# Kernel optimization log

Hardware: AMD Instinct MI355X
Metric: run time of the kernel (lower is better)

Reference implementation:

```python
import jax, jax.numpy as jnp
import numpy as np

E = 1024      # embed_dim (== embed_dim_)
NH = 8        # num_heads
HD = E // NH  # head_dim
BS1 = 2048
BS2 = 2048
EPS = 1e-5


def _layernorm(x, g, b):
    m = jnp.mean(x, axis=-1, keepdims=True)
    v = jnp.mean(jnp.square(x - m), axis=-1, keepdims=True)
    return (x - m) * jax.lax.rsqrt(v + EPS) * g + b


def setup_inputs() -> dict:
    key = jax.random.key(0)
    ks = jax.random.split(key, 16)
    s = 1.0 / np.sqrt(E)
    s4 = 1.0 / np.sqrt(4 * E)
    inp = {
        "x1": jax.random.normal(ks[0], (BS1, E), jnp.float32),
        "x2": jax.random.normal(ks[1], (BS2, E), jnp.float32),
        "Wq": jax.random.uniform(ks[2], (E, E), jnp.float32, -s, s),
        "bq": jax.random.uniform(ks[3], (E,), jnp.float32, -s, s),
        "Wk": jax.random.uniform(ks[4], (E, E), jnp.float32, -s, s),
        "bk": jax.random.uniform(ks[5], (E,), jnp.float32, -s, s),
        "Wv": jax.random.uniform(ks[6], (E, E), jnp.float32, -s, s),
        "bv": jax.random.uniform(ks[7], (E,), jnp.float32, -s, s),
        "Wo": jax.random.uniform(ks[8], (E, E), jnp.float32, -s, s),
        "bo": jax.random.uniform(ks[9], (E,), jnp.float32, -s, s),
        "W1": jax.random.uniform(ks[10], (4 * E, E), jnp.float32, -s, s),
        "b1": jax.random.uniform(ks[11], (4 * E,), jnp.float32, -s, s),
        "W2": jax.random.uniform(ks[12], (E, 4 * E), jnp.float32, -s4, s4),
        "b2": jax.random.uniform(ks[13], (E,), jnp.float32, -s4, s4),
        "g1": jnp.ones((E,), jnp.float32),
        "be1": jnp.zeros((E,), jnp.float32),
        "g2": jnp.ones((E,), jnp.float32),
        "be2": jnp.zeros((E,), jnp.float32),
    }
    return inp


def reference(x1, x2, Wq, bq, Wk, bk, Wv, bv, Wo, bo, W1, b1, W2, b2, g1, be1, g2, be2):
    scale = HD ** -0.5
    # Projections; attention runs over the batch axis (n=bs1, m=bs2)
    q = (x1 @ Wq.T + bq).reshape(BS1, NH, HD)   # [n,h,d]
    k = (x2 @ Wk.T + bk).reshape(BS2, NH, HD)   # [m,h,d]
    v = (x2 @ Wv.T + bv).reshape(BS2, NH, HD)   # [m,h,d]
    scores = jnp.einsum('nhd,mhd->nmh', q, k) * scale  # [n,m,h]
    # NOTE: faithful to source: softmax over the HEADS axis (dim=-1)
    probs = jax.nn.softmax(scores, axis=-1)
    # dropout is identity in eval mode
    attn = jnp.einsum('nmh,mhd->nhd', probs, v).reshape(BS1, E)
    attn = attn @ Wo.T + bo
    h = _layernorm(x1 + attn, g1, be1)
    ffn = jax.nn.relu(h @ W1.T + b1) @ W2.T + b2
    return _layernorm(h + ffn, g2, be2)
```

## Files before the change

### kernel.cpp

```cpp
#include <hip/hip_runtime.h>

#define BS 2048
#define EMB 1024
#define NHEAD 8
#define HDIM 128

typedef unsigned short u16;
typedef __attribute__((ext_vector_type(8))) short bf16x8;
typedef __attribute__((ext_vector_type(4))) float f32x4;

__device__ __forceinline__ u16 f32_bf16(float f) {
  unsigned u = __float_as_uint(f);
  u += 0x7fffu + ((u >> 16) & 1u);
  return (u16)(u >> 16);
}
__device__ __forceinline__ float bf2f(u16 x) {
  return __uint_as_float((unsigned)x << 16);
}

__device__ __forceinline__ void gld_lds16(const void* g, void* l) {
  __builtin_amdgcn_global_load_lds(
      (const __attribute__((address_space(1))) void*)g,
      (__attribute__((address_space(3))) void*)l, 16, 0, 0);
}

struct CvtArgs { const float* src[8]; };
__global__ __launch_bounds__(256) void cvt_all(CvtArgs a, u16* __restrict__ dst) {
  long i = (long)blockIdx.x * 256 + threadIdx.x;
  int seg = (int)(i >> 18);
  const float* src; long b;
  if (seg < 2)       { src = a.src[0]; b = 0; }
  else if (seg < 4)  { src = a.src[1]; b = 2L << 18; }
  else if (seg == 4) { src = a.src[2]; b = 4L << 18; }
  else if (seg == 5) { src = a.src[3]; b = 5L << 18; }
  else if (seg == 6) { src = a.src[4]; b = 6L << 18; }
  else if (seg == 7) { src = a.src[5]; b = 7L << 18; }
  else if (seg < 12) { src = a.src[6]; b = 8L << 18; }
  else               { src = a.src[7]; b = 12L << 18; }
  float4 v = ((const float4*)src)[i - b];
  ushort4 o;
  o.x = f32_bf16(v.x); o.y = f32_bf16(v.y); o.z = f32_bf16(v.z); o.w = f32_bf16(v.w);
  ((ushort4*)dst)[i] = o;
}

__device__ __forceinline__ void gemm_core(
    const u16* __restrict__ A, const u16* __restrict__ B, void* __restrict__ Cp,
    const float* __restrict__ bias, int K, int lda, int ldb, int ldc,
    long cbase, int mode, int relu, int m0, int n0) {
  __shared__ __align__(16) u16 As[128 * 32];
  __shared__ __align__(16) u16 Bs[128 * 32];
  const int t = threadIdx.x;
  const int lane = t & 63, l15 = lane & 15, quad = lane >> 4;
  const int wv = t >> 6, wr = wv & 1, wc = wv >> 1;
  const int wbase = t & ~63;

  f32x4 acc[4][4];
#pragma unroll
  for (int r = 0; r < 4; ++r)
#pragma unroll
    for (int c = 0; c < 4; ++c) acc[r][c] = (f32x4){0.f, 0.f, 0.f, 0.f};

  for (int k0 = 0; k0 < K; k0 += 32) {
#pragma unroll
    for (int i = 0; i < 2; ++i) {
      int s = i * 256 + t;
      gld_lds16(A + (long)(m0 + (s >> 2)) * lda + k0 + (s & 3) * 8,
                As + (i * 256 + wbase) * 8);
    }
#pragma unroll
    for (int i = 0; i < 2; ++i) {
      int s = i * 256 + t;
      gld_lds16(B + (long)(n0 + (s >> 2)) * ldb + k0 + (s & 3) * 8,
                Bs + (i * 256 + wbase) * 8);
    }
    __syncthreads();
    bf16x8 fa[4], fb[4];
#pragma unroll
    for (int r = 0; r < 4; ++r)
      fa[r] = *(const bf16x8*)&As[(wr * 64 + r * 16 + l15) * 32 + quad * 8];
#pragma unroll
    for (int c = 0; c < 4; ++c)
      fb[c] = *(const bf16x8*)&Bs[(wc * 64 + c * 16 + l15) * 32 + quad * 8];
#pragma unroll
    for (int r = 0; r < 4; ++r)
#pragma unroll
      for (int c = 0; c < 4; ++c)
        acc[r][c] = __builtin_amdgcn_mfma_f32_16x16x32_bf16(fa[r], fb[c], acc[r][c], 0, 0, 0);
    __syncthreads();
  }

#pragma unroll
  for (int r = 0; r < 4; ++r)
#pragma unroll
    for (int c = 0; c < 4; ++c) {
      const int m = m0 + wr * 64 + r * 16 + quad * 4;
      const int n = n0 + wc * 64 + c * 16 + l15;
      const float bv = bias ? bias[n] : 0.f;
      f32x4 v = acc[r][c];
      if (mode == 2) {
        ushort4 o;
        o.x = f32_bf16(v[0] + bv);
        o.y = f32_bf16(v[1] + bv);
        o.z = f32_bf16(v[2] + bv);
        o.w = f32_bf16(v[3] + bv);
        *(ushort4*)((u16*)Cp + cbase + (long)n * ldc + m) = o;
      } else {
#pragma unroll
        for (int i = 0; i < 4; ++i) {
          float x = v[i] + bv;
          if (relu) x = fmaxf(x, 0.f);
          if (mode == 0)
            ((float*)Cp)[cbase + (long)(m + i) * ldc + n] = x;
          else
            ((u16*)Cp)[cbase + (long)(m + i) * ldc + n] = f32_bf16(x);
        }
      }
    }
}

__global__ __launch_bounds__(256) void gemm_bt_k(
    const u16* __restrict__ A, const u16* __restrict__ B, void* __restrict__ C,
    const float* __restrict__ bias, int K, int lda, int ldb, int ldc,
    long aOffZ, long bOffZ, long cOffZ, int mode, int relu) {
  gemm_core(A + (long)blockIdx.z * aOffZ, B + (long)blockIdx.z * bOffZ, C, bias,
            K, lda, ldb, ldc, (long)blockIdx.z * cOffZ, mode, relu,
            blockIdx.y * 128, blockIdx.x * 128);
}

__global__ __launch_bounds__(256) void qkv_kernel(
    const u16* __restrict__ x1b, const u16* __restrict__ x2b,
    const u16* __restrict__ Wqb, const u16* __restrict__ Wkb, const u16* __restrict__ Wvb,
    const float* __restrict__ bq, const float* __restrict__ bk, const float* __restrict__ bv,
    u16* __restrict__ Qb, u16* __restrict__ Kb, u16* __restrict__ Vt) {
  const int z = blockIdx.z;
  const u16* A = (z == 0) ? x1b : x2b;
  const u16* B = (z == 0) ? Wqb : (z == 1) ? Wkb : Wvb;
  void* C = (z == 0) ? (void*)Qb : (z == 1) ? (void*)Kb : (void*)Vt;
  const float* bias = (z == 0) ? bq : (z == 1) ? bk : bv;
  const int mode = (z == 2) ? 2 : 1;
  const int ldc = (z == 2) ? 2048 : 1024;
  gemm_core(A, B, C, bias, 1024, 1024, 1024, ldc, 0, mode, 0,
            blockIdx.y * 128, blockIdx.x * 128);
}

__global__ __launch_bounds__(512, 2) void attn_fused(
    const u16* __restrict__ Q, const u16* __restrict__ Km, const u16* __restrict__ Vt,
    u16* __restrict__ p0, u16* __restrict__ p1, u16* __restrict__ p2, u16* __restrict__ p3) {
  __shared__ __align__(16) u16 Qs[32 * 1024];
  __shared__ __align__(16) u16 Ps[8 * 32 * 128];
  const int t = threadIdx.x;
  const int lane = t & 63, l15 = lane & 15, quad = lane >> 4;
  const int w = t >> 6, wbase = t & ~63;
  const int n0 = blockIdx.x * 32;
  const int mz = blockIdx.y * 512;
  u16* part = (blockIdx.y == 0) ? p0 : (blockIdx.y == 1) ? p1 : (blockIdx.y == 2) ? p2 : p3;

#pragma unroll
  for (int i = 0; i < 8; ++i) {
    int s = i * 512 + t;
    int n = s >> 7;
    int kel = (((s & 127) << 3) ^ ((n & 7) << 3));
    gld_lds16(Q + (long)(n0 + n) * 1024 + kel, Qs + (i * 512 + wbase) * 8);
  }

  f32x4 accp[2][8];
#pragma unroll
  for (int r = 0; r < 2; ++r)
#pragma unroll
    for (int c = 0; c < 8; ++c) accp[r][c] = (f32x4){0.f, 0.f, 0.f, 0.f};

  for (int it = 0; it < 4; ++it) {
    __syncthreads();
    f32x4 accs[8][2];
#pragma unroll
    for (int h = 0; h < 8; ++h)
#pragma unroll
      for (int c = 0; c < 2; ++c) accs[h][c] = (f32x4){0.f, 0.f, 0.f, 0.f};
    const u16* krow = Km + (long)(mz + it * 128 + w * 16 + l15) * 1024;
#pragma unroll
    for (int h = 0; h < 8; ++h)
#pragma unroll
      for (int kk = 0; kk < 4; ++kk) {
        bf16x8 kf = *(const bf16x8*)&krow[h * 128 + kk * 32 + quad * 8];
#pragma unroll
        for (int c = 0; c < 2; ++c) {
          int n = c * 16 + l15;
          int kel = (h * 128 + kk * 32 + quad * 8) ^ ((n & 7) << 3);
          bf16x8 qf = *(const bf16x8*)&Qs[n * 1024 + kel];
          accs[h][c] = __builtin_amdgcn_mfma_f32_16x16x32_bf16(kf, qf, accs[h][c], 0, 0, 0);
        }
      }
    const float scale = 0.08838834764831845f;
#pragma unroll
    for (int c = 0; c < 2; ++c)
#pragma unroll
      for (int i = 0; i < 4; ++i) {
        float mx = accs[0][c][i];
#pragma unroll
        for (int h = 1; h < 8; ++h) mx = fmaxf(mx, accs[h][c][i]);
        float sum = 0.f;
#pragma unroll
        for (int h = 0; h < 8; ++h) {
          float e = __expf((accs[h][c][i] - mx) * scale);
          accs[h][c][i] = e;
          sum += e;
        }
        float inv = 1.f / sum;
#pragma unroll
        for (int h = 0; h < 8; ++h) accs[h][c][i] *= inv;
      }
#pragma unroll
    for (int h = 0; h < 8; ++h)
#pragma unroll
      for (int c = 0; c < 2; ++c) {
        int n = c * 16 + l15;
        ushort4 o;
        o.x = f32_bf16(accs[h][c][0]);
        o.y = f32_bf16(accs[h][c][1]);
        o.z = f32_bf16(accs[h][c][2]);
        o.w = f32_bf16(accs[h][c][3]);
        int mb = (w * 32 + quad * 8) ^ ((n & 7) << 4);
        *(ushort4*)((char*)Ps + h * 8192 + n * 256 + mb) = o;
      }
    __syncthreads();
#pragma unroll
    for (int mq = 0; mq < 4; ++mq) {
      bf16x8 pa[2];
#pragma unroll
      for (int r = 0; r < 2; ++r) {
        int n = r * 16 + l15;
        int mb = (mq * 64 + quad * 16) ^ ((n & 7) << 4);
        pa[r] = *(const bf16x8*)((const char*)Ps + w * 8192 + n * 256 + mb);
      }
#pragma unroll
      for (int c = 0; c < 8; ++c) {
        bf16x8 vf = *(const bf16x8*)&Vt[(long)(w * 128 + c * 16 + l15) * 2048 +
                                        mz + it * 128 + mq * 32 + quad * 8];
#pragma unroll
        for (int r = 0; r < 2; ++r)
          accp[r][c] = __builtin_amdgcn_mfma_f32_16x16x32_bf16(pa[r], vf, accp[r][c], 0, 0, 0);
      }
    }
  }
#pragma unroll
  for (int r = 0; r < 2; ++r)
#pragma unroll
    for (int c = 0; c < 8; ++c)
#pragma unroll
      for (int i = 0; i < 4; ++i)
        part[(long)(n0 + r * 16 + quad * 4 + i) * 1024 + w * 128 + c * 16 + l15] =
            f32_bf16(accp[r][c][i]);
}

__global__ __launch_bounds__(256) void reduce4p_bf16(
    const u16* __restrict__ p0, const u16* __restrict__ p1,
    const u16* __restrict__ p2, const u16* __restrict__ p3, u16* __restrict__ out) {
  long i = (long)blockIdx.x * 256 + threadIdx.x;
  ushort4 a = ((const ushort4*)p0)[i];
  ushort4 b = ((const ushort4*)p1)[i];
  ushort4 c = ((const ushort4*)p2)[i];
  ushort4 d = ((const ushort4*)p3)[i];
  ushort4 o;
  o.x = f32_bf16(bf2f(a.x) + bf2f(b.x) + bf2f(c.x) + bf2f(d.x));
  o.y = f32_bf16(bf2f(a.y) + bf2f(b.y) + bf2f(c.y) + bf2f(d.y));
  o.z = f32_bf16(bf2f(a.z) + bf2f(b.z) + bf2f(c.z) + bf2f(d.z));
  o.w = f32_bf16(bf2f(a.w) + bf2f(b.w) + bf2f(c.w) + bf2f(d.w));
  ((ushort4*)out)[i] = o;
}

__global__ __launch_bounds__(256) void ln_residual_p4(
    const float* __restrict__ x,
    const u16* __restrict__ p0, const u16* __restrict__ p1,
    const u16* __restrict__ p2, const u16* __restrict__ p3,
    const float* __restrict__ colb, const float* __restrict__ g, const float* __restrict__ b,
    float* __restrict__ out32, u16* __restrict__ out16) {
  const int row = blockIdx.x, t = threadIdx.x;
  const long base = (long)row * EMB;
  float4 v = ((const float4*)(x + base))[t];
  ushort4 a0 = ((const ushort4*)(p0 + base))[t];
  ushort4 a1 = ((const ushort4*)(p1 + base))[t];
  ushort4 a2 = ((const ushort4*)(p2 + base))[t];
  ushort4 a3 = ((const ushort4*)(p3 + base))[t];
  float4 cb = ((const float4*)colb)[t];
  v.x += bf2f(a0.x) + bf2f(a1.x) + bf2f(a2.x) + bf2f(a3.x) + cb.x;
  v.y += bf2f(a0.y) + bf2f(a1.y) + bf2f(a2.y) + bf2f(a3.y) + cb.y;
  v.z += bf2f(a0.z) + bf2f(a1.z) + bf2f(a2.z) + bf2f(a3.z) + cb.z;
  v.w += bf2f(a0.w) + bf2f(a1.w) + bf2f(a2.w) + bf2f(a3.w) + cb.w;
  float s = v.x + v.y + v.z + v.w;
  float q = v.x * v.x + v.y * v.y + v.z * v.z + v.w * v.w;
#pragma unroll
  for (int off = 32; off > 0; off >>= 1) {
    s += __shfl_xor(s, off);
    q += __shfl_xor(q, off);
  }
  __shared__ float red[8];
  const int wv = t >> 6, lane = t & 63;
  if (lane == 0) { red[wv] = s; red[4 + wv] = q; }
  __syncthreads();
  s = red[0] + red[1] + red[2] + red[3];
  q = red[4] + red[5] + red[6] + red[7];
  const float mean = s * (1.f / EMB);
  const float var = q * (1.f / EMB) - mean * mean;
  const float rstd = rsqrtf(var + 1e-5f);
  float4 gg = ((const float4*)g)[t];
  float4 bb = ((const float4*)b)[t];
  float4 o;
  o.x = (v.x - mean) * rstd * gg.x + bb.x;
  o.y = (v.y - mean) * rstd * gg.y + bb.y;
  o.z = (v.z - mean) * rstd * gg.z + bb.z;
  o.w = (v.w - mean) * rstd * gg.w + bb.w;
  ((float4*)(out32 + base))[t] = o;
  if (out16) {
    ushort4 ho;
    ho.x = f32_bf16(o.x); ho.y = f32_bf16(o.y); ho.z = f32_bf16(o.z); ho.w = f32_bf16(o.w);
    ((ushort4*)(out16 + base))[t] = ho;
  }
}

extern "C" void kernel_launch(void* const* d_in, const int* in_sizes, int n_in,
                              void* d_out, int out_size, void* d_ws, size_t ws_size,
                              hipStream_t stream) {
  const float* x1 = (const float*)d_in[0];
  const float* x2 = (const float*)d_in[1];
  const float* Wq = (const float*)d_in[2];
  const float* bq = (const float*)d_in[3];
  const float* Wk = (const float*)d_in[4];
  const float* bk = (const float*)d_in[5];
  const float* Wv = (const float*)d_in[6];
  const float* bv = (const float*)d_in[7];
  const float* Wo = (const float*)d_in[8];
  const float* bo = (const float*)d_in[9];
  const float* W1 = (const float*)d_in[10];
  const float* b1 = (const float*)d_in[11];
  const float* W2 = (const float*)d_in[12];
  const float* b2 = (const float*)d_in[13];
  const float* g1 = (const float*)d_in[14];
  const float* be1 = (const float*)d_in[15];
  const float* g2 = (const float*)d_in[16];
  const float* be2 = (const float*)d_in[17];

  char* ws = (char*)d_ws;
  const size_t MB = 1ull << 20;
  u16* x1b = (u16*)(ws + 0 * MB);
  u16* x2b = (u16*)(ws + 4 * MB);
  u16* Wqb = (u16*)(ws + 8 * MB);
  u16* Wkb = (u16*)(ws + 10 * MB);
  u16* Wvb = (u16*)(ws + 12 * MB);
  u16* Wob = (u16*)(ws + 14 * MB);
  u16* W1b = (u16*)(ws + 16 * MB);
  u16* W2b = (u16*)(ws + 24 * MB);
  u16* Qb  = (u16*)(ws + 32 * MB);
  u16* Kb  = (u16*)(ws + 36 * MB);
  u16* Vtb = (u16*)(ws + 40 * MB);
  u16* attnb = (u16*)(ws + 44 * MB);
  u16* aP[4] = {(u16*)(ws + 48 * MB), (u16*)(ws + 52 * MB),
                (u16*)(ws + 56 * MB), (u16*)(ws + 60 * MB)};
  u16* woP[4] = {(u16*)(ws + 48 * MB), (u16*)(ws + 52 * MB),
                 (u16*)(ws + 56 * MB), (u16*)(ws + 60 * MB)};
  float* h32  = (float*)(ws + 64 * MB);
  u16*  h16   = (u16*)(ws + 72 * MB);
  u16*  ffn1b = (u16*)(ws + 76 * MB);
  u16* f2P[4] = {(u16*)(ws + 92 * MB), (u16*)(ws + 96 * MB),
                 (u16*)(ws + 100 * MB), (u16*)(ws + 104 * MB)};

  CvtArgs ca;
  ca.src[0] = x1; ca.src[1] = x2; ca.src[2] = Wq; ca.src[3] = Wk;
  ca.src[4] = Wv; ca.src[5] = Wo; ca.src[6] = W1; ca.src[7] = W2;
  cvt_all<<<16384, 256, 0, stream>>>(ca, (u16*)ws);

  qkv_kernel<<<dim3(8, 16, 3), 256, 0, stream>>>(x1b, x2b, Wqb, Wkb, Wvb, bq, bk, bv, Qb, Kb, Vtb);

  attn_fused<<<dim3(64, 4), 512, 0, stream>>>(Qb, Kb, Vtb, aP[0], aP[1], aP[2], aP[3]);

  reduce4p_bf16<<<2048, 256, 0, stream>>>(aP[0], aP[1], aP[2], aP[3], attnb);

  gemm_bt_k<<<dim3(8, 16, 4), 256, 0, stream>>>(attnb, Wob, woP[0], nullptr,
                                                256, 1024, 1024, 1024,
                                                256, 256, (long)BS * 1024, 1, 0);

  ln_residual_p4<<<2048, 256, 0, stream>>>(x1, woP[0], woP[1], woP[2], woP[3],
                                           bo, g1, be1, h32, h16);

  gemm_bt_k<<<dim3(32, 16, 1), 256, 0, stream>>>(h16, W1b, ffn1b, b1,
                                                 1024, 1024, 1024, 4096,
                                                 0, 0, 0, 1, 1);

  gemm_bt_k<<<dim3(8, 16, 4), 256, 0, stream>>>(ffn1b, W2b, f2P[0], nullptr,
                                                1024, 4096, 4096, 1024,
                                                1024, 1024, (long)BS * 1024, 1, 0);

  ln_residual_p4<<<2048, 256, 0, stream>>>(h32, f2P[0], f2P[1], f2P[2], f2P[3],
                                           b2, g2, be2, (float*)d_out, nullptr);
}
```

Measured before the change: 336.4 us.

## Split attention n-rows across twice as many waves per block

Launches the fused attention kernel with 1024 threads, so each of 16 waves handles 16 query rows for one m-slice instead of 32 rows. This halves per-wave accumulator registers and doubles waves per CU to improve latency hiding. In exchange, K and V fragments are fetched redundantly by both row-halves, and the aggressive launch bound may constrain register allocation.

```diff
diff --git a/kernel.cpp b/kernel.cpp
--- a/kernel.cpp
+++ b/kernel.cpp
@@ -143,7 +143,7 @@
             blockIdx.y * 128, blockIdx.x * 128);
 }
 
-__global__ __launch_bounds__(512, 2) void attn_fused(
+__global__ __launch_bounds__(1024, 4) void attn_fused(
     const u16* __restrict__ Q, const u16* __restrict__ Km, const u16* __restrict__ Vt,
     u16* __restrict__ p0, u16* __restrict__ p1, u16* __restrict__ p2, u16* __restrict__ p3) {
   __shared__ __align__(16) u16 Qs[32 * 1024];
@@ -151,105 +151,86 @@
   const int t = threadIdx.x;
   const int lane = t & 63, l15 = lane & 15, quad = lane >> 4;
   const int w = t >> 6, wbase = t & ~63;
+  const int mw = w & 7, nh = w >> 3;
   const int n0 = blockIdx.x * 32;
   const int mz = blockIdx.y * 512;
   u16* part = (blockIdx.y == 0) ? p0 : (blockIdx.y == 1) ? p1 : (blockIdx.y == 2) ? p2 : p3;
 
 #pragma unroll
-  for (int i = 0; i < 8; ++i) {
-    int s = i * 512 + t;
+  for (int i = 0; i < 4; ++i) {
+    int s = i * 1024 + t;
     int n = s >> 7;
     int kel = (((s & 127) << 3) ^ ((n & 7) << 3));
-    gld_lds16(Q + (long)(n0 + n) * 1024 + kel, Qs + (i * 512 + wbase) * 8);
-  }
-
-  f32x4 accp[2][8];
-#pragma unroll
-  for (int r = 0; r < 2; ++r)
-#pragma unroll
-    for (int c = 0; c < 8; ++c) accp[r][c] = (f32x4){0.f, 0.f, 0.f, 0.f};
+    gld_lds16(Q + (long)(n0 + n) * 1024 + kel, Qs + (i * 1024 + wbase) * 8);
+  }
+
+  const int nq = nh * 16 + l15;
+  const int swz3 = (nq & 7) << 3;
+  const int swz4 = (nq & 7) << 4;
+
+  f32x4 accp[8];
+#pragma unroll
+  for (int c = 0; c < 8; ++c) accp[c] = (f32x4){0.f, 0.f, 0.f, 0.f};
 
   for (int it = 0; it < 4; ++it) {
     __syncthreads();
-    f32x4 accs[8][2];
-#pragma unroll
-    for (int h = 0; h < 8; ++h)
-#pragma unroll
-      for (int c = 0; c < 2; ++c) accs[h][c] = (f32x4){0.f, 0.f, 0.f, 0.f};
-    const u16* krow = Km + (long)(mz + it * 128 + w * 16 + l15) * 1024;
+    f32x4 accs[8];
+#pragma unroll
+    for (int h = 0; h < 8; ++h) accs[h] = (f32x4){0.f, 0.f, 0.f, 0.f};
+    const u16* krow = Km + (long)(mz + it * 128 + mw * 16 + l15) * 1024;
 #pragma unroll
     for (int h = 0; h < 8; ++h)
 #pragma unroll
       for (int kk = 0; kk < 4; ++kk) {
         bf16x8 kf = *(const bf16x8*)&krow[h * 128 + kk * 32 + quad * 8];
-#pragma unroll
-        for (int c = 0; c < 2; ++c) {
-          int n = c * 16 + l15;
-          int kel = (h * 128 + kk * 32 + quad * 8) ^ ((n & 7) << 3);
-          bf16x8 qf = *(const bf16x8*)&Qs[n * 1024 + kel];
-          accs[h][c] = __builtin_amdgcn_mfma_f32_16x16x32_bf16(kf, qf, accs[h][c], 0, 0, 0);
-        }
+        bf16x8 qf = *(const bf16x8*)&Qs[nq * 1024 + ((h * 128 + kk * 32 + quad * 8) ^ swz3)];
+        accs[h] = __builtin_amdgcn_mfma_f32_16x16x32_bf16(kf, qf, accs[h], 0, 0, 0);
       }
     const float scale = 0.08838834764831845f;
 #pragma unroll
-    for (int c = 0; c < 2; ++c)
-#pragma unroll
-      for (int i = 0; i < 4; ++i) {
-        float mx = accs[0][c][i];
-#pragma unroll
-        for (int h = 1; h < 8; ++h) mx = fmaxf(mx, accs[h][c][i]);
-        float sum = 0.f;
-#pragma unroll
-        for (int h = 0; h < 8; ++h) {
-          float e = __expf((accs[h][c][i] - mx) * scale);
-          accs[h][c][i] = e;
-          sum += e;
-        }
-        float inv = 1.f / sum;
-#pragma unroll
-        for (int h = 0; h < 8; ++h) accs[h][c][i] *= inv;
+    for (int i = 0; i < 4; ++i) {
+      float mx = accs[0][i];
+#pragma unroll
+      for (int h = 1; h < 8; ++h) mx = fmaxf(mx, accs[h][i]);
+      float sum = 0.f;
+#pragma unroll
+      for (int h = 0; h < 8; ++h) {
+        float e = __expf((accs[h][i] - mx) * scale);
+        accs[h][i] = e;
+        sum += e;
       }
-#pragma unroll
-    for (int h = 0; h < 8; ++h)
-#pragma unroll
-      for (int c = 0; c < 2; ++c) {
-        int n = c * 16 + l15;
-        ushort4 o;
-        o.x = f32_bf16(accs[h][c][0]);
-        o.y = f32_bf16(accs[h][c][1]);
-        o.z = f32_bf16(accs[h][c][2]);
-        o.w = f32_bf16(accs[h][c][3]);
-        int mb = (w * 32 + quad * 8) ^ ((n & 7) << 4);
-        *(ushort4*)((char*)Ps + h * 8192 + n * 256 + mb) = o;
+      float inv = 1.f / sum;
+#pragma unroll
+      for (int h = 0; h < 8; ++h) accs[h][i] *= inv;
+    }
+#pragma unroll
+    for (int h = 0; h < 8; ++h) {
+      ushort4 o;
+      o.x = f32_bf16(accs[h][0]);
+      o.y = f32_bf16(accs[h][1]);
+      o.z = f32_bf16(accs[h][2]);
+      o.w = f32_bf16(accs[h][3]);
+      *(ushort4*)((char*)Ps + h * 8192 + nq * 256 + ((mw * 32 + quad * 8) ^ swz4)) = o;
+    }
+    __syncthreads();
+#pragma unroll
+    for (int mq = 0; mq < 4; ++mq) {
+      bf16x8 pa = *(const bf16x8*)((const char*)Ps + mw * 8192 + nq * 256 +
+                                   ((mq * 64 + quad * 16) ^ swz4));
+      const u16* vb = Vt + (long)(mw * 128) * 2048 + mz + it * 128 + mq * 32 + quad * 8;
+#pragma unroll
+      for (int c = 0; c < 8; ++c) {
+        bf16x8 vf = *(const bf16x8*)&vb[(long)(c * 16 + l15) * 2048];
+        accp[c] = __builtin_amdgcn_mfma_f32_16x16x32_bf16(pa, vf, accp[c], 0, 0, 0);
       }
-    __syncthreads();
-#pragma unroll
-    for (int mq = 0; mq < 4; ++mq) {
-      bf16x8 pa[2];
-#pragma unroll
-      for (int r = 0; r < 2; ++r) {
-        int n = r * 16 + l15;
-        int mb = (mq * 64 + quad * 16) ^ ((n & 7) << 4);
-        pa[r] = *(const bf16x8*)((const char*)Ps + w * 8192 + n * 256 + mb);
-      }
-#pragma unroll
-      for (int c = 0; c < 8; ++c) {
-        bf16x8 vf = *(const bf16x8*)&Vt[(long)(w * 128 + c * 16 + l15) * 2048 +
-                                        mz + it * 128 + mq * 32 + quad * 8];
-#pragma unroll
-        for (int r = 0; r < 2; ++r)
-          accp[r][c] = __builtin_amdgcn_mfma_f32_16x16x32_bf16(pa[r], vf, accp[r][c], 0, 0, 0);
-      }
-    }
-  }
-#pragma unroll
-  for (int r = 0; r < 2; ++r)
-#pragma unroll
-    for (int c = 0; c < 8; ++c)
-#pragma unroll
-      for (int i = 0; i < 4; ++i)
-        part[(long)(n0 + r * 16 + quad * 4 + i) * 1024 + w * 128 + c * 16 + l15] =
-            f32_bf16(accp[r][c][i]);
+    }
+  }
+#pragma unroll
+  for (int c = 0; c < 8; ++c)
+#pragma unroll
+    for (int i = 0; i < 4; ++i)
+      part[(long)(n0 + nh * 16 + quad * 4 + i) * 1024 + mw * 128 + c * 16 + l15] =
+          f32_bf16(accp[c][i]);
 }
 
 __global__ __launch_bounds__(256) void reduce4p_bf16(
@@ -370,7 +351,7 @@
 
   qkv_kernel<<<dim3(8, 16, 3), 256, 0, stream>>>(x1b, x2b, Wqb, Wkb, Wvb, bq, bk, bv, Qb, Kb, Vtb);
 
-  attn_fused<<<dim3(64, 4), 512, 0, stream>>>(Qb, Kb, Vtb, aP[0], aP[1], aP[2], aP[3]);
+  attn_fused<<<dim3(64, 4), 1024, 0, stream>>>(Qb, Kb, Vtb, aP[0], aP[1], aP[2], aP[3]);
 
   reduce4p_bf16<<<2048, 256, 0, stream>>>(aP[0], aP[1], aP[2], aP[3], attnb);
 
```

Result: slower. 389.5 us (+15.8%).

## Stage K tiles through LDS per head pair and batch V loads ahead of MFMAs

Applied to the files above, without the earlier changes.

The score phase now streams K tiles (128 rows x 2 heads) and matching Q slices into swizzled LDS with async global-to-LDS loads, in four head-pair stages. This replaces the full 32x1024 Q staging and the direct per-lane global K reads. In the PV phase, all eight V fragments are loaded before the MFMAs so the global loads are in flight together. The aim is coalesced K access and better latency hiding, at the cost of extra __syncthreads per stage with no double buffering, more LDS, and more registers.

```diff
diff --git a/kernel.cpp b/kernel.cpp
--- a/kernel.cpp
+++ b/kernel.cpp
@@ -146,7 +146,8 @@
 __global__ __launch_bounds__(512, 2) void attn_fused(
     const u16* __restrict__ Q, const u16* __restrict__ Km, const u16* __restrict__ Vt,
     u16* __restrict__ p0, u16* __restrict__ p1, u16* __restrict__ p2, u16* __restrict__ p3) {
-  __shared__ __align__(16) u16 Qs[32 * 1024];
+  __shared__ __align__(16) u16 Ks[2][128][128];
+  __shared__ __align__(16) u16 Qs[2][32][128];
   __shared__ __align__(16) u16 Ps[8 * 32 * 128];
   const int t = threadIdx.x;
   const int lane = t & 63, l15 = lane & 15, quad = lane >> 4;
@@ -155,14 +156,6 @@
   const int mz = blockIdx.y * 512;
   u16* part = (blockIdx.y == 0) ? p0 : (blockIdx.y == 1) ? p1 : (blockIdx.y == 2) ? p2 : p3;
 
-#pragma unroll
-  for (int i = 0; i < 8; ++i) {
-    int s = i * 512 + t;
-    int n = s >> 7;
-    int kel = (((s & 127) << 3) ^ ((n & 7) << 3));
-    gld_lds16(Q + (long)(n0 + n) * 1024 + kel, Qs + (i * 512 + wbase) * 8);
-  }
-
   f32x4 accp[2][8];
 #pragma unroll
   for (int r = 0; r < 2; ++r)
@@ -170,26 +163,47 @@
     for (int c = 0; c < 8; ++c) accp[r][c] = (f32x4){0.f, 0.f, 0.f, 0.f};
 
   for (int it = 0; it < 4; ++it) {
-    __syncthreads();
+    const int mb = mz + it * 128;
     f32x4 accs[8][2];
 #pragma unroll
     for (int h = 0; h < 8; ++h)
 #pragma unroll
       for (int c = 0; c < 2; ++c) accs[h][c] = (f32x4){0.f, 0.f, 0.f, 0.f};
-    const u16* krow = Km + (long)(mz + it * 128 + w * 16 + l15) * 1024;
-#pragma unroll
-    for (int h = 0; h < 8; ++h)
-#pragma unroll
-      for (int kk = 0; kk < 4; ++kk) {
-        bf16x8 kf = *(const bf16x8*)&krow[h * 128 + kk * 32 + quad * 8];
-#pragma unroll
-        for (int c = 0; c < 2; ++c) {
-          int n = c * 16 + l15;
-          int kel = (h * 128 + kk * 32 + quad * 8) ^ ((n & 7) << 3);
-          bf16x8 qf = *(const bf16x8*)&Qs[n * 1024 + kel];
-          accs[h][c] = __builtin_amdgcn_mfma_f32_16x16x32_bf16(kf, qf, accs[h][c], 0, 0, 0);
+
+#pragma unroll
+    for (int hs = 0; hs < 4; ++hs) {
+      __syncthreads();
+#pragma unroll
+      for (int i = 0; i < 8; ++i) {
+        int s = i * 512 + t;
+        int hh = s >> 11, m = (s >> 4) & 127, g = s & 15;
+        gld_lds16(Km + (long)(mb + m) * 1024 + (hs * 2 + hh) * 128 + ((g * 8) ^ ((m & 7) << 3)),
+                  (u16*)Ks + (i * 512 + wbase) * 8);
+      }
+#pragma unroll
+      for (int i = 0; i < 2; ++i) {
+        int s = i * 512 + t;
+        int hh = s >> 9, n = (s >> 4) & 31, g = s & 15;
+        gld_lds16(Q + (long)(n0 + n) * 1024 + (hs * 2 + hh) * 128 + ((g * 8) ^ ((n & 7) << 3)),
+                  (u16*)Qs + (i * 512 + wbase) * 8);
+      }
+      __syncthreads();
+#pragma unroll
+      for (int hh = 0; hh < 2; ++hh)
+#pragma unroll
+        for (int kk = 0; kk < 4; ++kk) {
+          const int m = w * 16 + l15;
+          bf16x8 fa = *(const bf16x8*)&Ks[hh][m][(kk * 32 + quad * 8) ^ ((m & 7) << 3)];
+#pragma unroll
+          for (int c = 0; c < 2; ++c) {
+            const int n = c * 16 + l15;
+            bf16x8 fb = *(const bf16x8*)&Qs[hh][n][(kk * 32 + quad * 8) ^ ((n & 7) << 3)];
+            accs[hs * 2 + hh][c] =
+                __builtin_amdgcn_mfma_f32_16x16x32_bf16(fa, fb, accs[hs * 2 + hh][c], 0, 0, 0);
+          }
         }
-      }
+    }
+
     const float scale = 0.08838834764831845f;
 #pragma unroll
     for (int c = 0; c < 2; ++c)
@@ -219,27 +233,28 @@
         o.y = f32_bf16(accs[h][c][1]);
         o.z = f32_bf16(accs[h][c][2]);
         o.w = f32_bf16(accs[h][c][3]);
-        int mb = (w * 32 + quad * 8) ^ ((n & 7) << 4);
-        *(ushort4*)((char*)Ps + h * 8192 + n * 256 + mb) = o;
+        *(ushort4*)((char*)Ps + h * 8192 + n * 256 + ((w * 32 + quad * 8) ^ ((n & 7) << 4))) = o;
       }
     __syncthreads();
 #pragma unroll
     for (int mq = 0; mq < 4; ++mq) {
+      bf16x8 vf[8];
+#pragma unroll
+      for (int c = 0; c < 8; ++c)
+        vf[c] = *(const bf16x8*)&Vt[(long)(w * 128 + c * 16 + l15) * 2048 +
+                                    mb + mq * 32 + quad * 8];
       bf16x8 pa[2];
 #pragma unroll
       for (int r = 0; r < 2; ++r) {
         int n = r * 16 + l15;
-        int mb = (mq * 64 + quad * 16) ^ ((n & 7) << 4);
-        pa[r] = *(const bf16x8*)((const char*)Ps + w * 8192 + n * 256 + mb);
-      }
-#pragma unroll
-      for (int c = 0; c < 8; ++c) {
-        bf16x8 vf = *(const bf16x8*)&Vt[(long)(w * 128 + c * 16 + l15) * 2048 +
-                                        mz + it * 128 + mq * 32 + quad * 8];
+        pa[r] = *(const bf16x8*)((const char*)Ps + w * 8192 + n * 256 +
+                                 ((mq * 64 + quad * 16) ^ ((n & 7) << 4)));
+      }
+#pragma unroll
+      for (int c = 0; c < 8; ++c)
 #pragma unroll
         for (int r = 0; r < 2; ++r)
-          accp[r][c] = __builtin_amdgcn_mfma_f32_16x16x32_bf16(pa[r], vf, accp[r][c], 0, 0, 0);
-      }
+          accp[r][c] = __builtin_amdgcn_mfma_f32_16x16x32_bf16(pa[r], vf[c], accp[r][c], 0, 0, 0);
     }
   }
 #pragma unroll
```

Result: no change. 335.9 us (-0.1%).
